# Performance work log

Measured on AMD Instinct MI355X. Metric: run time of the kernel, lower is better.

## Reference

```python
import jax, jax.numpy as jnp
import numpy as np

H, DH, RK, RD = 16, 128, 512, 64  # num_heads, head_dim, kv_lora_rank, rope_dim


def apply_rope(x, cos, sin):
    # x: [..., L, ..., rope_dim]; cos/sin: [L, rope_dim//2]
    cos = cos[None, :, None, :]
    sin = sin[None, :, None, :]
    x1, x2 = x[..., 0::2], x[..., 1::2]
    out_real = x1 * cos - x2 * sin
    out_imag = x1 * sin + x2 * cos
    return jnp.stack([out_real, out_imag], axis=-1).reshape(x.shape)


def setup_inputs() -> dict:
    key = jax.random.key(0)
    ks = jax.random.split(key, 7)
    B, L, E, MAXLEN = 2, 2048, 2048, 4096
    x = jax.random.normal(ks[0], (B, L, E), dtype=jnp.float32)
    cos_table = jax.random.uniform(ks[1], (MAXLEN, RD // 2), dtype=jnp.float32)
    sin_table = jax.random.uniform(ks[2], (MAXLEN, RD // 2), dtype=jnp.float32)
    wq = jax.random.normal(ks[3], (E, H * (DH + RD)), dtype=jnp.float32) / np.sqrt(E)
    wkv_down = jax.random.normal(ks[4], (E, RK + RD), dtype=jnp.float32) / np.sqrt(E)
    w_up = jax.random.normal(ks[5], (RK, H * (2 * DH + RD)), dtype=jnp.float32) / np.sqrt(RK)
    w_out = jax.random.normal(ks[6], (H * (DH + RD), E), dtype=jnp.float32) / np.sqrt(H * (DH + RD))
    return {"x": x, "cos_table": cos_table, "sin_table": sin_table,
            "wq": wq, "wkv_down": wkv_down, "w_up": w_up, "w_out": w_out}


def reference(x, cos_table, sin_table, wq, wkv_down, w_up, w_out):
    # Prefill path (use_cache=False): idx = 0, kv comes from current tokens only.
    B, L, E = x.shape
    cos = cos_table[:L]
    sin = sin_table[:L]

    # Queries: per-head content part + rope part
    q_all = (x @ wq).reshape(B, L, H, DH + RD)
    q_head, q_rope = q_all[..., :DH], q_all[..., DH:]
    q_rope = apply_rope(q_rope, cos, sin)
    q = jnp.concatenate([q_head, q_rope], axis=-1)  # [B,L,H,DH+RD]

    # Compressed KV latent + shared rope key
    kv_lat = x @ wkv_down                            # [B,L,RK+RD]
    c_kv = kv_lat[..., :RK]
    k_rope = kv_lat[..., RK:]
    k_rope = apply_rope(k_rope[:, :, None, :], cos, sin)[:, :, 0, :]  # [B,L,RD]

    # Up-project latent to per-head K/V
    up = (c_kv @ w_up).reshape(B, L, H, 2 * DH + RD)
    k_head = up[..., :DH]
    v_head = up[..., DH:2 * DH]
    v_rope = up[..., 2 * DH:]
    k_rope_b = jnp.broadcast_to(k_rope[:, :, None, :], (B, L, H, RD))
    k = jnp.concatenate([k_head, k_rope_b], axis=-1)  # [B,L,H,DH+RD]
    v = jnp.concatenate([v_head, v_rope], axis=-1)    # [B,L,H,DH+RD]

    # Causal attention (query_indices = arange(L), key_indices = arange(L))
    scale = 1.0 / jnp.sqrt(jnp.float32(DH + RD))
    scores = jnp.einsum('blhd,bshd->bhls', q, k) * scale
    idxs = jnp.arange(L)
    bias = jnp.where(idxs[:, None] >= idxs[None, :], 0.0, -1000000000.0)
    attn = jax.nn.softmax(scores + bias[None, None, :, :], axis=-1)
    out = jnp.einsum('bhls,bshd->blhd', attn, v)  # [B,L,H,DH+RD]
    return out.reshape(B, L, -1) @ w_out
```

## Files before the change

### kernel.cpp

```cpp
#include <hip/hip_runtime.h>
#include <stdint.h>

#define H_ 16
#define DH_ 128
#define RK_ 512
#define RD_ 64
#define B_ 2
#define L_ 2048
#define E_ 2048
#define DQ_ 192
#define NQ_ (H_*DQ_)
#define NKV_ 576
#define NKVP_ 640
#define NQKV_ 3712
#define NUP_ (H_*(2*DH_+RD_))
#define M_ (B_*L_)

typedef unsigned short u16;
typedef __bf16 bf16x8 __attribute__((ext_vector_type(8)));
typedef float floatx4 __attribute__((ext_vector_type(4)));

__device__ __forceinline__ u16 f2bf(float f) {
    union { float f; uint32_t u; } v; v.f = f;
    uint32_t u = v.u;
    u = (u + 0x7fffu + ((u >> 16) & 1u)) >> 16;
    return (u16)u;
}
__device__ __forceinline__ float bf2f(u16 b) {
    union { uint32_t u; float f; } v; v.u = ((uint32_t)b) << 16; return v.f;
}

__device__ __forceinline__ void gld_lds16(const void* g, void* l) {
    __builtin_amdgcn_global_load_lds((__attribute__((address_space(1))) void*)(g),
                                     (__attribute__((address_space(3))) void*)(l),
                                     16, 0, 0);
}

__global__ void convert_bf16(const float* __restrict__ in, u16* __restrict__ out, int n4) {
    int i = blockIdx.x * blockDim.x + threadIdx.x;
    if (i >= n4) return;
    float4 v = ((const float4*)in)[i];
    uint2 o;
    o.x = (uint32_t)f2bf(v.x) | ((uint32_t)f2bf(v.y) << 16);
    o.y = (uint32_t)f2bf(v.z) | ((uint32_t)f2bf(v.w) << 16);
    ((uint2*)out)[i] = o;
}

__global__ void transpose_w(const float* __restrict__ W, u16* __restrict__ Wt,
                            int K, int N, int Npad) {
    __shared__ float tile[32][33];
    int n0 = blockIdx.x * 32, k0 = blockIdx.y * 32;
    int tx = threadIdx.x, ty = threadIdx.y;
    for (int i = 0; i < 4; i++) {
        int k = k0 + ty + i * 8, n = n0 + tx;
        tile[ty + i * 8][tx] = (n < N) ? W[(size_t)k * N + n] : 0.f;
    }
    __syncthreads();
    for (int i = 0; i < 4; i++) {
        int n = n0 + ty + i * 8, k = k0 + tx;
        Wt[(size_t)n * K + k] = f2bf(tile[tx][ty + i * 8]);
    }
}

__global__ __launch_bounds__(256) void gemm_bt(const u16* __restrict__ A,
                                               const u16* __restrict__ Bt,
                                               float* __restrict__ C,
                                               int M, int N, int K) {
    __shared__ __align__(16) u16 As[128 * 32];
    __shared__ __align__(16) u16 Bs[128 * 32];
    const int tid = threadIdx.x;
    const int wave = tid >> 6, lane = tid & 63;
    const int quad = lane >> 4, l16 = lane & 15;
    const int m0 = blockIdx.y * 128, n0 = blockIdx.x * 128;
    const int wm = (wave >> 1) * 64, wn = (wave & 1) * 64;

    floatx4 zero4 = {0.f, 0.f, 0.f, 0.f};
    floatx4 acc[4][4];
    for (int i = 0; i < 4; i++) for (int j = 0; j < 4; j++) acc[i][j] = zero4;

    const u16* Ab = A + (size_t)m0 * K;
    const u16* Bb = Bt + (size_t)n0 * K;

    for (int k0 = 0; k0 < K; k0 += 32) {
        for (int it = 0; it < 2; ++it) {
            int c = it * 256 + tid;
            int row = c >> 2, cr = c & 3;
            gld_lds16(Ab + (size_t)row * K + k0 + cr * 8, As + c * 8);
            gld_lds16(Bb + (size_t)row * K + k0 + cr * 8, Bs + c * 8);
        }
        __syncthreads();
        bf16x8 af[4], bfr[4];
        for (int i = 0; i < 4; i++) af[i]  = *(const bf16x8*)(As + (wm + i * 16 + l16) * 32 + quad * 8);
        for (int j = 0; j < 4; j++) bfr[j] = *(const bf16x8*)(Bs + (wn + j * 16 + l16) * 32 + quad * 8);
        for (int i = 0; i < 4; i++)
            for (int j = 0; j < 4; j++)
                acc[i][j] = __builtin_amdgcn_mfma_f32_16x16x32_bf16(af[i], bfr[j], acc[i][j], 0, 0, 0);
        __syncthreads();
    }
    for (int i = 0; i < 4; i++)
        for (int j = 0; j < 4; j++) {
            int mrow = m0 + wm + i * 16 + quad * 4;
            int ncol = n0 + wn + j * 16 + l16;
            float* Cp = C + (size_t)mrow * N + ncol;
            for (int r = 0; r < 4; r++) Cp[(size_t)r * N] = acc[i][j][r];
        }
}

__global__ void build_q(const float* __restrict__ qkv, const float* __restrict__ cosT,
                        const float* __restrict__ sinT, u16* __restrict__ qb) {
    const float QS = 0.07216878364870323f * 1.4426950408889634f;
    int idx = blockIdx.x * blockDim.x + threadIdx.x;
    if (idx >= M_ * H_ * 96) return;
    int p = idx % 96; int t = idx / 96; int h = t % H_; int row = t / H_;
    int l = row & (L_ - 1); int b = row >> 11;
    const float* src = qkv + (size_t)row * NQKV_ + h * DQ_;
    u16* dst = qb + ((size_t)(b * H_ + h) * L_ + l) * DQ_;
    int d = 2 * p;
    float x1 = src[d], x2 = src[d + 1];
    if (d < DH_) { dst[d] = f2bf(x1 * QS); dst[d + 1] = f2bf(x2 * QS); }
    else {
        int i = (d - DH_) >> 1;
        float c = cosT[(size_t)l * 32 + i], s = sinT[(size_t)l * 32 + i];
        dst[d]     = f2bf((x1 * c - x2 * s) * QS);
        dst[d + 1] = f2bf((x1 * s + x2 * c) * QS);
    }
}

__global__ void build_ckv(const float* __restrict__ qkv, const float* __restrict__ cosT,
                          const float* __restrict__ sinT, u16* __restrict__ ckv,
                          u16* __restrict__ kropeb) {
    int idx = blockIdx.x * blockDim.x + threadIdx.x;
    if (idx >= M_ * 288) return;
    int j = idx % 288; int row = idx / 288;
    int l = row & (L_ - 1);
    const float* src = qkv + (size_t)row * NQKV_ + NQ_;
    if (j < 256) {
        ckv[(size_t)row * RK_ + 2 * j]     = f2bf(src[2 * j]);
        ckv[(size_t)row * RK_ + 2 * j + 1] = f2bf(src[2 * j + 1]);
    } else {
        int i = j - 256;
        float x1 = src[RK_ + 2 * i], x2 = src[RK_ + 2 * i + 1];
        float c = cosT[(size_t)l * 32 + i], s = sinT[(size_t)l * 32 + i];
        kropeb[(size_t)row * RD_ + 2 * i]     = f2bf(x1 * c - x2 * s);
        kropeb[(size_t)row * RD_ + 2 * i + 1] = f2bf(x1 * s + x2 * c);
    }
}

__global__ __launch_bounds__(256) void build_kvt(const float* __restrict__ up,
        const u16* __restrict__ kropeb, u16* __restrict__ kb, u16* __restrict__ vtb) {
    __shared__ float vt[64][193];
    int blk = blockIdx.x;
    int lt = blk & 31; int bh = blk >> 5; int h = bh % H_; int b = bh / H_;
    int tid = threadIdx.x;
    int l0 = lt * 64;
    for (int it = 0; it < 48; ++it) {
        int idx = it * 256 + tid;
        int lr = idx / 192, d = idx % 192;
        size_t row = (size_t)b * L_ + l0 + lr;
        float vv = (d < DH_) ? up[row * NUP_ + h * 320 + DH_ + d]
                             : up[row * NUP_ + h * 320 + 2 * DH_ + (d - DH_)];
        vt[lr][d] = vv;
        u16 kbf = (d < DH_) ? f2bf(up[row * NUP_ + h * 320 + d])
                            : kropeb[row * RD_ + (d - DH_)];
        kb[((size_t)bh * L_ + l0 + lr) * DQ_ + d] = kbf;
    }
    __syncthreads();
    for (int it = 0; it < 48; ++it) {
        int idx = it * 256 + tid;
        int lr = idx & 63, d = idx >> 6;
        int l = l0 + lr;
        int s5 = l & 31;
        int k5 = ((s5 >> 2) & 3) * 8 + ((s5 >> 4) & 1) * 4 + (s5 & 3);
        int lp = (l & ~31) | k5;
        vtb[((size_t)bh * DQ_ + d) * L_ + lp] = f2bf(vt[lr][d]);
    }
}

__global__ __launch_bounds__(512, 2) void attn(const u16* __restrict__ qb,
        const u16* __restrict__ kb, const u16* __restrict__ vtb,
        u16* __restrict__ po0, u16* __restrict__ po1,
        float* __restrict__ pm0, float* __restrict__ pl0,
        float* __restrict__ pm1, float* __restrict__ pl1) {
    __shared__ __align__(16) u16 Ks[2][64 * 192];
    __shared__ __align__(16) u16 Vs[2][192 * 64];
    int id = blockIdx.x;
    int bh = id & 31, tj = id >> 5;
    int t = tj >> 1, j = tj & 1;
    int tid = threadIdx.x, wave = tid >> 6, lane = tid & 63;
    int quad = lane >> 4, l16 = lane & 15;

    const int x7 = l16 & 7;
    const int h2 = (x7 >> 2) & 1;
    const int qx = quad ^ (x7 & 3);
    const int oA = h2 * 32 + qx * 8;
    const int oB = (1 - h2) * 32 + qx * 8;

    u16* po = j ? po1 : po0;
    float* pm = j ? pm1 : pm0;
    float* pl = j ? pl1 : pl0;

    const u16* kbase0 = kb + (size_t)bh * L_ * DQ_;
    const u16* vbase0 = vtb + (size_t)bh * (size_t)DQ_ * L_;
    floatx4 zero4 = {0.f, 0.f, 0.f, 0.f};

    auto stageKV = [&](int st, int buf) {
        const u16* kg = kbase0 + (size_t)st * 64 * DQ_;
        u16* kd = &Ks[buf][0];
        for (int it = 0; it < 3; ++it) {
            int c = it * 512 + tid;
            int s = c / 24, blk = c - s * 24;
            int blog = (blk & 24) | ((blk & 7) ^ (s & 7));
            gld_lds16(kg + (size_t)s * DQ_ + blog * 8, kd + c * 8);
        }
        const u16* vg = vbase0 + st * 64;
        u16* vd = &Vs[buf][0];
        for (int it = 0; it < 3; ++it) {
            int c = it * 512 + tid;
            int d = c >> 3, blk = c & 7;
            int blog = blk ^ (d & 7);
            gld_lds16(vg + (size_t)d * L_ + blog * 8, vd + c * 8);
        }
    };

    for (int seg = 0; seg < 2; ++seg) {
        const int QT = seg == 0 ? (7 - t) : t;
        const int st0 = j ? (2 * QT + 2) : 0;
        const int st1 = j ? (4 * QT + 3) : (2 * QT + 1);

        bf16x8 aq[2][6];
        const u16* qbase = qb + ((size_t)bh * L_ + QT * 256 + wave * 16 + l16) * DQ_;
        for (int a = 0; a < 2; a++)
            for (int kk = 0; kk < 6; kk++)
                aq[a][kk] = *(const bf16x8*)(qbase + a * 128 * DQ_ + kk * 32 + quad * 8);

        floatx4 o[2][12];
        for (int a = 0; a < 2; a++) for (int i = 0; i < 12; i++) o[a][i] = zero4;
        float m_i[2] = {-INFINITY, -INFINITY};
        float l_i[2] = {0.f, 0.f};

        int cur = 0;
        stageKV(st0, 0);

        for (int st = st0; st <= st1; ++st) {
            if (st < st1) {
                stageKV(st + 1, cur ^ 1);
                asm volatile("s_waitcnt vmcnt(6)" ::: "memory");
            } else {
                asm volatile("s_waitcnt vmcnt(0)" ::: "memory");
            }
            __builtin_amdgcn_s_barrier();
            const u16* Kc = &Ks[cur][0];
            const u16* Vc = &Vs[cur][0];

            int R0 = QT * 256 + wave * 16 - st * 64;
            int R1 = R0 + 128;
            int smax0 = min(3, (R0 + 15) >> 4);
            int smax1 = min(3, (R1 + 15) >> 4);
            bool live0 = smax0 >= 0, live1 = smax1 >= 0;

            float pv[2][4][4];
            float mxa[2] = {-INFINITY, -INFINITY};
#pragma unroll
            for (int stile = 0; stile < 4; ++stile) {
                if (stile > smax1) {
                    for (int r = 0; r < 4; r++) { pv[0][stile][r] = 0.f; pv[1][stile][r] = 0.f; }
                    continue;
                }
                bool do0 = (stile <= smax0);
                floatx4 s1v = zero4, s0v = zero4;
#pragma unroll
                for (int kk = 0; kk < 6; kk++) {
                    int off = (kk >> 1) * 64 + ((kk & 1) ? oB : oA);
                    bf16x8 kf = *(const bf16x8*)(Kc + (stile * 16 + l16) * 192 + off);
                    s1v = __builtin_amdgcn_mfma_f32_16x16x32_bf16(kf, aq[1][kk], s1v, 0, 0, 0);
                    if (do0) s0v = __builtin_amdgcn_mfma_f32_16x16x32_bf16(kf, aq[0][kk], s0v, 0, 0, 0);
                }
                int sb = stile * 16;
                if (sb + 15 > R1) {
                    for (int r = 0; r < 4; r++) {
                        float v = (sb + quad * 4 + r > R1 + l16) ? -1e30f : s1v[r];
                        pv[1][stile][r] = v; mxa[1] = fmaxf(mxa[1], v);
                    }
                } else {
                    for (int r = 0; r < 4; r++) { pv[1][stile][r] = s1v[r]; mxa[1] = fmaxf(mxa[1], s1v[r]); }
                }
                if (do0) {
                    if (sb + 15 > R0) {
                        for (int r = 0; r < 4; r++) {
                            float v = (sb + quad * 4 + r > R0 + l16) ? -1e30f : s0v[r];
                            pv[0][stile][r] = v; mxa[0] = fmaxf(mxa[0], v);
                        }
                    } else {
                        for (int r = 0; r < 4; r++) { pv[0][stile][r] = s0v[r]; mxa[0] = fmaxf(mxa[0], s0v[r]); }
                    }
                } else {
                    for (int r = 0; r < 4; r++) pv[0][stile][r] = 0.f;
                }
            }

            bf16x8 pf[2][2];
            bool lv[2] = {live0, live1};
            int smx[2] = {smax0, smax1};
#pragma unroll
            for (int a = 0; a < 2; a++) {
                if (!lv[a]) continue;
                float mx = mxa[a];
                mx = fmaxf(mx, __shfl_xor(mx, 16));
                mx = fmaxf(mx, __shfl_xor(mx, 32));
                float mn;
                if (__all(mx <= m_i[a] + 8.0f)) {
                    mn = m_i[a];
                } else {
                    mn = fmaxf(m_i[a], mx);
                    float alpha = exp2f(m_i[a] - mn);
                    m_i[a] = mn;
                    l_i[a] *= alpha;
                    for (int i = 0; i < 12; i++) o[a][i] *= alpha;
                }
                float rs = 0.f;
#pragma unroll
                for (int stile = 0; stile < 4; ++stile) {
                    if (stile > smx[a]) continue;
                    for (int r = 0; r < 4; r++) {
                        float e = exp2f(pv[a][stile][r] - mn);
                        pv[a][stile][r] = e;
                        rs += e;
                    }
                }
                rs += __shfl_xor(rs, 16);
                rs += __shfl_xor(rs, 32);
                l_i[a] += rs;
                for (int g = 0; g < 2; g++) {
                    union { bf16x8 v; u16 s[8]; } u;
                    for (int r = 0; r < 4; r++) {
                        u.s[r]     = f2bf(pv[a][g * 2][r]);
                        u.s[4 + r] = f2bf(pv[a][g * 2 + 1][r]);
                    }
                    pf[a][g] = u.v;
                }
            }

            for (int g = 0; g < 2; g++) {
                int vo = g ? oB : oA;
#pragma unroll
                for (int dtile = 0; dtile < 12; dtile++) {
                    bf16x8 vf = *(const bf16x8*)(Vc + (dtile * 16 + l16) * 64 + vo);
                    if (live0)
                        o[0][dtile] = __builtin_amdgcn_mfma_f32_16x16x32_bf16(vf, pf[0][g], o[0][dtile], 0, 0, 0);
                    if (live1)
                        o[1][dtile] = __builtin_amdgcn_mfma_f32_16x16x32_bf16(vf, pf[1][g], o[1][dtile], 0, 0, 0);
                }
            }
            __builtin_amdgcn_s_barrier();
            cur ^= 1;
        }

        int tile = bh * 8 + QT;
        for (int a = 0; a < 2; a++) {
            int q = a * 128 + wave * 16 + l16;
            u16* dst = po + ((size_t)tile * 256 + q) * 192;
            for (int dtile = 0; dtile < 12; dtile++) {
                ushort4 pk;
                pk.x = f2bf(o[a][dtile][0]);
                pk.y = f2bf(o[a][dtile][1]);
                pk.z = f2bf(o[a][dtile][2]);
                pk.w = f2bf(o[a][dtile][3]);
                *(ushort4*)(dst + dtile * 16 + quad * 4) = pk;
            }
            if (quad == 0) {
                pm[(size_t)tile * 256 + q] = m_i[a];
                pl[(size_t)tile * 256 + q] = l_i[a];
            }
        }
        __syncthreads();
    }
}

__global__ void attn_merge(const u16* __restrict__ po0, const u16* __restrict__ po1,
                           const float* __restrict__ pm0, const float* __restrict__ pl0,
                           const float* __restrict__ pm1, const float* __restrict__ pl1,
                           u16* __restrict__ ao) {
    int idx = blockIdx.x * blockDim.x + threadIdx.x;
    int c = idx % 48; int rest = idx / 48;
    int q = rest & 255; int tile = rest >> 8;
    int bh = tile >> 3, QT = tile & 7;
    size_t mi = (size_t)tile * 256 + q;
    float m0 = pm0[mi], m1 = pm1[mi];
    float l0 = pl0[mi], l1 = pl1[mi];
    float m = fmaxf(m0, m1);
    float a0 = exp2f(m0 - m), a1 = exp2f(m1 - m);
    float inv = 1.0f / (l0 * a0 + l1 * a1);
    float s0 = a0 * inv, s1 = a1 * inv;
    ushort4 u0 = *(const ushort4*)(po0 + mi * 192 + c * 4);
    ushort4 u1 = *(const ushort4*)(po1 + mi * 192 + c * 4);
    int b = bh >> 4, h = bh & 15;
    int l = QT * 256 + q;
    u16* dst = ao + (((size_t)(b * L_ + l)) * H_ + h) * DQ_ + c * 4;
    ushort4 pk;
    pk.x = f2bf(bf2f(u0.x) * s0 + bf2f(u1.x) * s1);
    pk.y = f2bf(bf2f(u0.y) * s0 + bf2f(u1.y) * s1);
    pk.z = f2bf(bf2f(u0.z) * s0 + bf2f(u1.z) * s1);
    pk.w = f2bf(bf2f(u0.w) * s0 + bf2f(u1.w) * s1);
    *(ushort4*)dst = pk;
}

extern "C" void kernel_launch(void* const* d_in, const int* in_sizes, int n_in,
                              void* d_out, int out_size, void* d_ws, size_t ws_size,
                              hipStream_t stream) {
    const float* x    = (const float*)d_in[0];
    const float* cosT = (const float*)d_in[1];
    const float* sinT = (const float*)d_in[2];
    const float* wq   = (const float*)d_in[3];
    const float* wkv  = (const float*)d_in[4];
    const float* wup  = (const float*)d_in[5];
    const float* wout = (const float*)d_in[6];
    float* out = (float*)d_out;
    char* ws = (char*)d_ws;

    size_t off = 0;
    auto alloc = [&](size_t b) { size_t r = off; off += (b + 255) & ~(size_t)255; return r; };
    u16* xb     = (u16*)(ws + alloc((size_t)M_ * E_ * 2));
    u16* wqkvT  = (u16*)(ws + alloc((size_t)NQKV_ * E_ * 2));
    u16* wupT   = (u16*)(ws + alloc((size_t)NUP_ * RK_ * 2));
    u16* woutT  = (u16*)(ws + alloc((size_t)E_ * NQ_ * 2));
    u16* qb     = (u16*)(ws + alloc((size_t)B_ * H_ * L_ * DQ_ * 2));
    u16* kb     = (u16*)(ws + alloc((size_t)B_ * H_ * L_ * DQ_ * 2));
    u16* vtb    = (u16*)(ws + alloc((size_t)B_ * H_ * DQ_ * L_ * 2));
    u16* ao     = (u16*)(ws + alloc((size_t)M_ * NQ_ * 2));
    u16* ckv    = (u16*)(ws + alloc((size_t)M_ * RK_ * 2));
    u16* kropeb = (u16*)(ws + alloc((size_t)M_ * RD_ * 2));
    char* scratch = ws + alloc((size_t)M_ * NUP_ * 4);
    float* qkv = (float*)(scratch);
    float* up  = (float*)(scratch);
    size_t poSz = (size_t)256 * 256 * 192 * 2;
    u16*   po0 = (u16*)(scratch);
    u16*   po1 = (u16*)(scratch + poSz);
    float* pm0 = (float*)(scratch + 2 * poSz);
    float* pl0 = (float*)(scratch + 2 * poSz + 256 * 256 * 4);
    float* pm1 = (float*)(scratch + 2 * poSz + 2 * 256 * 256 * 4);
    float* pl1 = (float*)(scratch + 2 * poSz + 3 * 256 * 256 * 4);

    dim3 tb(32, 8);
    int n4 = M_ * E_ / 4;
    convert_bf16<<<(n4 + 255) / 256, 256, 0, stream>>>(x, xb, n4);
    transpose_w<<<dim3(NQ_ / 32, E_ / 32), tb, 0, stream>>>(wq, wqkvT, E_, NQ_, NQ_);
    transpose_w<<<dim3(NKVP_ / 32, E_ / 32), tb, 0, stream>>>(wkv, wqkvT + (size_t)NQ_ * E_, E_, NKV_, NKVP_);
    transpose_w<<<dim3(NUP_ / 32, RK_ / 32), tb, 0, stream>>>(wup, wupT, RK_, NUP_, NUP_);
    transpose_w<<<dim3(E_ / 32, NQ_ / 32), tb, 0, stream>>>(wout, woutT, NQ_, E_, E_);

    gemm_bt<<<dim3(NQKV_ / 128, M_ / 128), 256, 0, stream>>>(xb, wqkvT, qkv, M_, NQKV_, E_);

    int nq = M_ * H_ * 96;
    build_q<<<(nq + 255) / 256, 256, 0, stream>>>(qkv, cosT, sinT, qb);
    int nc = M_ * 288;
    build_ckv<<<(nc + 255) / 256, 256, 0, stream>>>(qkv, cosT, sinT, ckv, kropeb);

    gemm_bt<<<dim3(NUP_ / 128, M_ / 128), 256, 0, stream>>>(ckv, wupT, up, M_, NUP_, RK_);
    build_kvt<<<B_ * H_ * 32, 256, 0, stream>>>(up, kropeb, kb, vtb);

    attn<<<256, 512, 0, stream>>>(qb, kb, vtb, po0, po1, pm0, pl0, pm1, pl1);
    attn_merge<<<(256 * 256 * 48) / 256, 256, 0, stream>>>(po0, po1, pm0, pl0, pm1, pl1, ao);

    gemm_bt<<<dim3(E_ / 128, M_ / 128), 256, 0, stream>>>(ao, woutT, out, M_, E_, NQ_);
}
```

Measured before the change: 617.0 us.

## Add 256x256 triple-buffered GEMM with XCD remap for QKV and output projections

Introduces a new GEMM kernel with 256x256 tiles, 512 threads, a three-stage async global-to-LDS pipeline, a swizzled LDS layout, and XCD-aware workgroup remapping. It replaces the 128x128 GEMM for the QKV and output projections. The QKV weight padding grows to 3840 so the N dimension divides by 256. The larger tiles raise data reuse and cut LDS traffic per MFMA, but use more registers and produce fewer workgroups (240 and 128), which may leave the 256 CUs underfilled.

Result: no change. 620.7 us (+0.6%).

```diff
diff --git a/kernel.cpp b/kernel.cpp
--- a/kernel.cpp
+++ b/kernel.cpp
@@ -12,7 +12,7 @@
 #define NQ_ (H_*DQ_)
 #define NKV_ 576
 #define NKVP_ 640
-#define NQKV_ 3712
+#define QKVP_ 3840
 #define NUP_ (H_*(2*DH_+RD_))
 #define M_ (B_*L_)
 
@@ -106,6 +106,93 @@
         }
 }
 
+__global__ __launch_bounds__(512, 2) void gemm256(const u16* __restrict__ A,
+                                                  const u16* __restrict__ Bt,
+                                                  float* __restrict__ C,
+                                                  int M, int N, int K) {
+    __shared__ __align__(16) u16 As[3][256 * 32];
+    __shared__ __align__(16) u16 Bs[3][256 * 32];
+    const int tid = threadIdx.x;
+    const int wave = tid >> 6, lane = tid & 63;
+    const int quad = lane >> 4, l16 = lane & 15;
+    const int wm = (wave >> 2) * 128, wn = (wave & 3) * 64;
+
+    int nwg = gridDim.x * gridDim.y;
+    int flat = blockIdx.y * gridDim.x + blockIdx.x;
+    int q = nwg >> 3, r = nwg & 7;
+    int xcd = flat & 7, pos = flat >> 3;
+    int wg = (xcd < r) ? xcd * (q + 1) + pos : r * (q + 1) + (xcd - r) * q + pos;
+    const int m0 = (wg & 15) * 256;
+    const int n0 = (wg >> 4) * 256;
+
+    const u16* Ab = A + (size_t)m0 * K;
+    const u16* Bb = Bt + (size_t)n0 * K;
+
+    const int srow = tid >> 2;
+    const int sblk = (((tid & 3) ^ ((tid >> 3) & 3))) * 8;
+    const int sdst = srow * 32 + (tid & 3) * 8;
+    const int qsw  = (quad ^ ((l16 >> 1) & 3)) * 8;
+
+    floatx4 zero4 = {0.f, 0.f, 0.f, 0.f};
+    floatx4 acc[8][4];
+#pragma unroll
+    for (int i = 0; i < 8; i++)
+#pragma unroll
+        for (int j = 0; j < 4; j++) acc[i][j] = zero4;
+
+    auto stage = [&](int t, int b) {
+        const u16* Ak = Ab + t * 32;
+        const u16* Bk = Bb + t * 32;
+        gld_lds16(Ak + (size_t)srow * K + sblk,         As[b] + sdst);
+        gld_lds16(Ak + (size_t)(srow + 128) * K + sblk, As[b] + sdst + 128 * 32);
+        gld_lds16(Bk + (size_t)srow * K + sblk,         Bs[b] + sdst);
+        gld_lds16(Bk + (size_t)(srow + 128) * K + sblk, Bs[b] + sdst + 128 * 32);
+    };
+
+    const int NT = K >> 5;
+    stage(0, 0);
+    stage(1, 1);
+    int rb = 0;
+    for (int t = 0; t < NT; ++t) {
+        if (t + 2 < NT) {
+            stage(t + 2, rb ? rb - 1 : 2);
+            asm volatile("s_waitcnt vmcnt(8)" ::: "memory");
+        } else if (t + 1 < NT) {
+            asm volatile("s_waitcnt vmcnt(4)" ::: "memory");
+        } else {
+            asm volatile("s_waitcnt vmcnt(0)" ::: "memory");
+        }
+        __builtin_amdgcn_s_barrier();
+
+        const u16* Ar = As[rb];
+        const u16* Br = Bs[rb];
+        bf16x8 af[8], bfv[4];
+#pragma unroll
+        for (int i = 0; i < 8; i++) af[i]  = *(const bf16x8*)(Ar + (wm + i * 16 + l16) * 32 + qsw);
+#pragma unroll
+        for (int j = 0; j < 4; j++) bfv[j] = *(const bf16x8*)(Br + (wn + j * 16 + l16) * 32 + qsw);
+        __builtin_amdgcn_s_setprio(1);
+#pragma unroll
+        for (int i = 0; i < 8; i++)
+#pragma unroll
+            for (int j = 0; j < 4; j++)
+                acc[i][j] = __builtin_amdgcn_mfma_f32_16x16x32_bf16(af[i], bfv[j], acc[i][j], 0, 0, 0);
+        __builtin_amdgcn_s_setprio(0);
+        __builtin_amdgcn_s_barrier();
+        rb = (rb == 2) ? 0 : rb + 1;
+    }
+
+#pragma unroll
+    for (int i = 0; i < 8; i++)
+#pragma unroll
+        for (int j = 0; j < 4; j++) {
+            int mrow = m0 + wm + i * 16 + quad * 4;
+            int ncol = n0 + wn + j * 16 + l16;
+            float* Cp = C + (size_t)mrow * N + ncol;
+            for (int rr = 0; rr < 4; rr++) Cp[(size_t)rr * N] = acc[i][j][rr];
+        }
+}
+
 __global__ void build_q(const float* __restrict__ qkv, const float* __restrict__ cosT,
                         const float* __restrict__ sinT, u16* __restrict__ qb) {
     const float QS = 0.07216878364870323f * 1.4426950408889634f;
@@ -113,7 +200,7 @@
     if (idx >= M_ * H_ * 96) return;
     int p = idx % 96; int t = idx / 96; int h = t % H_; int row = t / H_;
     int l = row & (L_ - 1); int b = row >> 11;
-    const float* src = qkv + (size_t)row * NQKV_ + h * DQ_;
+    const float* src = qkv + (size_t)row * QKVP_ + h * DQ_;
     u16* dst = qb + ((size_t)(b * H_ + h) * L_ + l) * DQ_;
     int d = 2 * p;
     float x1 = src[d], x2 = src[d + 1];
@@ -133,7 +220,7 @@
     if (idx >= M_ * 288) return;
     int j = idx % 288; int row = idx / 288;
     int l = row & (L_ - 1);
-    const float* src = qkv + (size_t)row * NQKV_ + NQ_;
+    const float* src = qkv + (size_t)row * QKVP_ + NQ_;
     if (j < 256) {
         ckv[(size_t)row * RK_ + 2 * j]     = f2bf(src[2 * j]);
         ckv[(size_t)row * RK_ + 2 * j + 1] = f2bf(src[2 * j + 1]);
@@ -420,7 +507,7 @@
     size_t off = 0;
     auto alloc = [&](size_t b) { size_t r = off; off += (b + 255) & ~(size_t)255; return r; };
     u16* xb     = (u16*)(ws + alloc((size_t)M_ * E_ * 2));
-    u16* wqkvT  = (u16*)(ws + alloc((size_t)NQKV_ * E_ * 2));
+    u16* wqkvT  = (u16*)(ws + alloc((size_t)QKVP_ * E_ * 2));
     u16* wupT   = (u16*)(ws + alloc((size_t)NUP_ * RK_ * 2));
     u16* woutT  = (u16*)(ws + alloc((size_t)E_ * NQ_ * 2));
     u16* qb     = (u16*)(ws + alloc((size_t)B_ * H_ * L_ * DQ_ * 2));
@@ -444,11 +531,11 @@
     int n4 = M_ * E_ / 4;
     convert_bf16<<<(n4 + 255) / 256, 256, 0, stream>>>(x, xb, n4);
     transpose_w<<<dim3(NQ_ / 32, E_ / 32), tb, 0, stream>>>(wq, wqkvT, E_, NQ_, NQ_);
-    transpose_w<<<dim3(NKVP_ / 32, E_ / 32), tb, 0, stream>>>(wkv, wqkvT + (size_t)NQ_ * E_, E_, NKV_, NKVP_);
+    transpose_w<<<dim3((QKVP_ - NQ_) / 32, E_ / 32), tb, 0, stream>>>(wkv, wqkvT + (size_t)NQ_ * E_, E_, NKV_, QKVP_ - NQ_);
     transpose_w<<<dim3(NUP_ / 32, RK_ / 32), tb, 0, stream>>>(wup, wupT, RK_, NUP_, NUP_);
     transpose_w<<<dim3(E_ / 32, NQ_ / 32), tb, 0, stream>>>(wout, woutT, NQ_, E_, E_);
 
-    gemm_bt<<<dim3(NQKV_ / 128, M_ / 128), 256, 0, stream>>>(xb, wqkvT, qkv, M_, NQKV_, E_);
+    gemm256<<<dim3(QKVP_ / 256, M_ / 256), 512, 0, stream>>>(xb, wqkvT, qkv, M_, QKVP_, E_);
 
     int nq = M_ * H_ * 96;
     build_q<<<(nq + 255) / 256, 256, 0, stream>>>(qkv, cosT, sinT, qb);
@@ -461,5 +548,5 @@
     attn<<<256, 512, 0, stream>>>(qb, kb, vtb, po0, po1, pm0, pl0, pm1, pl1);
     attn_merge<<<(256 * 256 * 48) / 256, 256, 0, stream>>>(po0, po1, pm0, pl0, pm1, pl1, ao);
 
-    gemm_bt<<<dim3(E_ / 128, M_ / 128), 256, 0, stream>>>(ao, woutT, out, M_, E_, NQ_);
-}
+    gemm256<<<dim3(E_ / 256, M_ / 256), 512, 0, stream>>>(ao, woutT, out, M_, E_, NQ_);
+}
```
